# Kernel tuning notes

Measured on AMD Instinct MI355X. Metric: run time of the kernel, lower is better.

## Reference

```python
import jax, jax.numpy as jnp
import numpy as np

B, T, D, E = 8, 2048, 256, 4
D_E = D // E


def setup_inputs() -> dict:
    key = jax.random.key(0)
    ks = jax.random.split(key, 12)
    s = 1.0 / np.sqrt(D)
    x = jax.random.normal(ks[0], (B, T, D), dtype=jnp.float32)
    # ensure max(seq_len) == T so the padded input matches this_batch_padlen
    seq_len = jnp.concatenate([
        jax.random.randint(ks[1], (B - 1,), T // 2, T),
        jnp.array([T]),
    ]).astype(jnp.int32)
    return {
        "x": x,
        "seq_len": seq_len,
        "wq": jax.random.uniform(ks[2], (D, D), jnp.float32, -s, s),
        "bq": jax.random.uniform(ks[3], (D,), jnp.float32, -s, s),
        "wk": jax.random.uniform(ks[4], (D, D), jnp.float32, -s, s),
        "bk": jax.random.uniform(ks[5], (D,), jnp.float32, -s, s),
        "wv": jax.random.uniform(ks[6], (D, D), jnp.float32, -s, s),
        "bv": jax.random.uniform(ks[7], (D,), jnp.float32, -s, s),
        "wo": jax.random.uniform(ks[8], (D, D), jnp.float32, -s, s),
        "bo": jax.random.uniform(ks[9], (D,), jnp.float32, -s, s),
        "theta": jnp.array([50.0], dtype=jnp.float32),
    }


def _split_heads(y):
    # faithful to torch: [B,T,D] -> permute(0,2,1) -> [B,D,T] -> reshape(B*E, T, D_E)
    return jnp.transpose(y, (0, 2, 1)).reshape(B * E, T, D_E)


def reference(x, seq_len, wq, bq, wk, bk, wv, bv, wo, bo, theta):
    Q = _split_heads(x @ wq.T + bq)          # [B*E, T, D_E]
    K = _split_heads(x @ wk.T + bk)          # [B*E, T, D_E]
    V = _split_heads(x @ wv.T + bv)          # [B*E, T, D_E]

    # padding mask: zero out query rows (and key cols) past seq_len[i]
    pos = jnp.arange(T)
    valid = (pos[None, :] < seq_len[:, None])                 # [B, T]
    mask_q = jnp.repeat(valid, E, axis=0).astype(Q.dtype)     # [B*E, T]
    Q = Q * mask_q[:, :, None]
    K = K * mask_q[:, :, None]

    scale = jnp.sqrt(jnp.float32(T))
    att = jnp.einsum('bqd,bkd->bqk', Q, K) / scale            # [B*E, T, T]

    # Gaussian positional penalty (is_punish=True)
    tpos = jnp.arange(T, dtype=jnp.float32)
    diff = tpos[None, :] - tpos[:, None]                      # j - i
    punish = jnp.exp(-(diff ** 2) / (theta[0] ** 2))          # [T, T]
    att = att * punish[None, :, :]

    att = jnp.where(att == 0.0, jnp.float32(-2e20), att)
    att = jax.nn.softmax(att, axis=2)

    ctx = jnp.einsum('bqk,bkd->bqd', att, V)                  # [B*E, T, D_E]
    # faithful inverse of _split_heads: permute(0,2,1)->reshape(B,D,T)->permute
    ctx = jnp.transpose(jnp.transpose(ctx, (0, 2, 1)).reshape(B, D, T), (0, 2, 1))
    A = ctx @ wo.T + bo
    return A + x
```

## Files before the change

### kernel.cpp

```cpp
#include <hip/hip_runtime.h>
#include <math.h>
#include <stdint.h>

#define B_SZ   8
#define T_SEQ  2048
#define DIM    256
#define NH     32
#define DE     64
#define BAND   509
#define M_ROWS (B_SZ * T_SEQ)

typedef __attribute__((ext_vector_type(8))) short short8;
typedef __attribute__((ext_vector_type(4))) float floatx4;
typedef unsigned short ushort_t;

__device__ __forceinline__ ushort_t f2bf(float x) {
    unsigned u = __float_as_uint(x);
    u += 0x7fffu + ((u >> 16) & 1u);
    return (ushort_t)(u >> 16);
}
__device__ __forceinline__ float bf2f(ushort_t b) {
    return __uint_as_float(((unsigned)b) << 16);
}
__device__ __forceinline__ unsigned pack2(float a, float b) {
    return (unsigned)f2bf(a) | ((unsigned)f2bf(b) << 16);
}

__device__ __forceinline__ double pd_exact(int d, float th) {
    float df  = (float)d;
    float arg = (-(df * df)) / (th * th);
    double pdd = exp((double)arg);
    if (pdd < 1.17549435082228751e-38)
        return rint(pdd * 0x1p149) * 0x1p-149;
    return (double)(float)pdd;
}

__global__ __launch_bounds__(256) void prep_kernel(
    const float* __restrict__ x,
    const float* __restrict__ wq, const float* __restrict__ wk,
    const float* __restrict__ wv, const float* __restrict__ wo,
    const float* __restrict__ theta,
    ushort_t* __restrict__ xb, ushort_t* __restrict__ wb,
    float* __restrict__ thr_g, float* __restrict__ pdf_g)
{
    const int bid = blockIdx.x, tid = threadIdx.x;
    if (bid < 2048) {
        size_t i8 = ((size_t)bid * 256 + tid) * 8;
        float4 a = *(const float4*)(x + i8);
        float4 b = *(const float4*)(x + i8 + 4);
        uint4 o;
        o.x = pack2(a.x, a.y); o.y = pack2(a.z, a.w);
        o.z = pack2(b.x, b.y); o.w = pack2(b.z, b.w);
        *(uint4*)(xb + i8) = o;
    } else if (bid < 2176) {
        size_t w8 = ((size_t)(bid - 2048) * 256 + tid) * 8;
        int which = (int)(w8 >> 16);
        const float* src = (which == 0) ? wq : (which == 1) ? wk : (which == 2) ? wv : wo;
        size_t off = w8 & 65535;
        float4 a = *(const float4*)(src + off);
        float4 b = *(const float4*)(src + off + 4);
        uint4 o;
        o.x = pack2(a.x, a.y); o.y = pack2(a.z, a.w);
        o.z = pack2(b.x, b.y); o.w = pack2(b.z, b.w);
        *(uint4*)(wb + w8) = o;
    } else {
        int i = (bid - 2176) * 256 + tid;
        float th = theta[0];
        if (i < 384) pdf_g[i] = (float)pd_exact(i, th);
        if (i < 288) {
            double pdv = pd_exact(321 + i, th);
            thr_g[i] = (pdv == 0.0) ? __builtin_inff() : (float)(0x1p-150 / pdv);
        }
    }
}

__global__ __launch_bounds__(256, 2) void proj_qkv_mfma(
    const ushort_t* __restrict__ xb, const ushort_t* __restrict__ wb,
    const float* __restrict__ bq, const float* __restrict__ bk,
    const float* __restrict__ bv, const int* __restrict__ seq_len,
    ushort_t* __restrict__ Qh, ushort_t* __restrict__ Kh, ushort_t* __restrict__ Vh)
{
    __shared__ __align__(16) ushort_t Ls[4][64][68];
    const int wave = threadIdx.x >> 6, lane = threadIdx.x & 63;
    const int quad = lane >> 4, l15 = lane & 15;
    const int task = blockIdx.x * 4 + wave;
    const int nt64 = task % 12;
    const int mstrip = task / 12;
    const int mode = nt64 >> 2;
    const int nloc_base = (nt64 & 3) * 64;
    const ushort_t* Wp = wb + (size_t)mode * 65536;
    const int m0 = mstrip * 64;
    const int bb = m0 >> 11;
    const int th0 = (m0 >> 6) & 31;
    const int sl = seq_len[bb];
    ushort_t* outp = (mode == 0) ? Qh : (mode == 1) ? Kh : Vh;
    const float* bias = (mode == 0) ? bq : (mode == 1) ? bk : bv;
    const int hh = bb * 4 + (nloc_base >> 6);
    const float oscale = (mode == 0) ? 0.022097086912079612f : 1.0f;

    short8 Bf[4][8];
    #pragma unroll
    for (int nt = 0; nt < 4; ++nt) {
        int nrow = nloc_base + nt * 16 + l15;
        #pragma unroll
        for (int ks = 0; ks < 8; ++ks)
            Bf[nt][ks] = *(const short8*)(Wp + (size_t)nrow * 256 + ks * 32 + quad * 8);
    }
    float bias4[4];
    #pragma unroll
    for (int nt = 0; nt < 4; ++nt) bias4[nt] = bias[nloc_base + nt * 16 + l15];

    short8 Acur[8];
    #pragma unroll
    for (int ks = 0; ks < 8; ++ks)
        Acur[ks] = *(const short8*)(xb + (size_t)(m0 + l15) * 256 + ks * 32 + quad * 8);

    #pragma unroll
    for (int mb = 0; mb < 4; ++mb) {
        const int mb0 = m0 + mb * 16;
        short8 Anext[8];
        if (mb < 3) {
            #pragma unroll
            for (int ks = 0; ks < 8; ++ks)
                Anext[ks] = *(const short8*)(xb + (size_t)(mb0 + 16 + l15) * 256 + ks * 32 + quad * 8);
        }
        floatx4 acc[4];
        #pragma unroll
        for (int nt = 0; nt < 4; ++nt) acc[nt] = (floatx4){0.f, 0.f, 0.f, 0.f};
        #pragma unroll
        for (int ks = 0; ks < 8; ++ks)
            #pragma unroll
            for (int nt = 0; nt < 4; ++nt)
                acc[nt] = __builtin_amdgcn_mfma_f32_16x16x32_bf16(Acur[ks], Bf[nt][ks], acc[nt], 0, 0, 0);
        #pragma unroll
        for (int nt = 0; nt < 4; ++nt) {
            float v0 = (acc[nt][0] + bias4[nt]) * oscale;
            float v1 = (acc[nt][1] + bias4[nt]) * oscale;
            float v2 = (acc[nt][2] + bias4[nt]) * oscale;
            float v3 = (acc[nt][3] + bias4[nt]) * oscale;
            uint2 pk; pk.x = pack2(v0, v1); pk.y = pack2(v2, v3);
            *(uint2*)&Ls[wave][nt * 16 + l15][mb * 16 + quad * 4] = pk;
        }
        #pragma unroll
        for (int ks = 0; ks < 8; ++ks) Acur[ks] = Anext[ks];
    }

    #pragma unroll
    for (int s = 0; s < 16; ++s) {
        int dl = s * 4 + quad;
        int e0 = l15 * 4;
        uint2 pk = *(const uint2*)&Ls[wave][dl][e0];
        int q = dl * 32 + th0;
        if (mode <= 1 && q >= sl) { pk.x = 0u; pk.y = 0u; }
        *(uint2*)(outp + (((size_t)hh * T_SEQ + q) << 6) + e0) = pk;
    }
}

__global__ __launch_bounds__(256) void vtrans_kernel(const ushort_t* __restrict__ Vh,
                                                     ushort_t* __restrict__ VTp)
{
    __shared__ ushort_t Vs[256][66];
    const int tid = threadIdx.x;
    const int h = blockIdx.x >> 3, chunk = blockIdx.x & 7;
    const ushort_t* src = Vh + ((size_t)(h * T_SEQ + chunk * 256)) * DE;
    #pragma unroll
    for (int rep = 0; rep < 8; ++rep) {
        int f = rep * 256 + tid;
        int row = f >> 3, c8 = (f & 7) * 8;
        *(uint4*)&Vs[row][c8] = *(const uint4*)(src + (size_t)row * DE + c8);
    }
    __syncthreads();
    const int w = tid >> 6, lane = tid & 63;
    const int half = lane >> 5;
    const int c32 = lane & 31;
    const int cbase = c32 * 8;
    const int blk = cbase >> 6;
    const int cin = cbase & 63;
    #pragma unroll
    for (int rr = 0; rr < 8; ++rr) {
        int e = w * 16 + rr * 2 + half;
        ushort_t tmp[8];
        #pragma unroll
        for (int t = 0; t < 8; ++t) {
            int ci = cin + t;
            int j = blk * 64 + (ci >> 2) + 16 * (ci & 3);
            tmp[t] = Vs[j][e];
        }
        *(uint4*)(VTp + ((size_t)(h * DE + e)) * T_SEQ + chunk * 256 + cbase) = *(uint4*)tmp;
    }
}

__global__ __launch_bounds__(256) void meanv_partial(const ushort_t* __restrict__ Vh,
                                                     float* __restrict__ mv) {
    __shared__ float red[32][72];
    const int blk = blockIdx.x;
    const int h = blk >> 3, chunk = blk & 7;
    const int tid = threadIdx.x;
    const int r0 = tid >> 3;
    const int es = (tid & 7) * 8;
    const ushort_t* p = Vh + ((size_t)h * T_SEQ + chunk * 256 + r0) * DE + es;
    float s[8] = {};
    #pragma unroll
    for (int k = 0; k < 8; ++k) {
        uint4 u = *(const uint4*)(p + (size_t)k * 32 * DE);
        const ushort_t* w = (const ushort_t*)&u;
        #pragma unroll
        for (int i = 0; i < 8; ++i) s[i] += bf2f(w[i]);
    }
    #pragma unroll
    for (int i = 0; i < 8; ++i) red[r0][es + i] = s[i];
    __syncthreads();
    if (tid < 64) {
        float t = 0.f;
        #pragma unroll
        for (int g = 0; g < 32; ++g) t += red[g][tid];
        atomicAdd(&mv[h * DE + tid], t);
    }
}

__global__ __launch_bounds__(256) void attn_mfma_kernel(
    const ushort_t* __restrict__ Qh, const ushort_t* __restrict__ Kh,
    const ushort_t* __restrict__ VTp, const float* __restrict__ thr_g,
    const float* __restrict__ pdf_g, const float* __restrict__ mvs,
    const int* __restrict__ seq_len, ushort_t* __restrict__ ctxb)
{
    __shared__ ushort_t Ks [64][72];
    __shared__ ushort_t VTs[64][72];
    __shared__ ushort_t Ps [4][16][72];
    __shared__ float pdfs[384];
    __shared__ float thrs[288];

    const int tid  = threadIdx.x;
    const int wave = tid >> 6;
    const int lane = tid & 63;
    const int quad = lane >> 4;
    const int l15  = lane & 15;
    const int bid   = blockIdx.x;
    const int inner = bid >> 3;
    const int h  = ((inner >> 5) << 3) | (bid & 7);
    const int q0 = (inner & 31) * 64;
    const int b  = h >> 2;
    const int sl = seq_len[b];
    const float invT = 1.0f / (float)T_SEQ;
    ushort_t* outbase = ctxb + ((size_t)b * T_SEQ + q0) * DIM + (size_t)(h & 3) * 64;

    if (q0 >= sl) {
        #pragma unroll
        for (int nt = 0; nt < 4; ++nt) {
            ushort_t mval = f2bf(mvs[h * DE + l15 + 16 * nt] * invT);
            #pragma unroll
            for (int r = 0; r < 4; ++r)
                outbase[(size_t)(wave * 16 + quad * 4 + r) * DIM + l15 + 16 * nt] = mval;
        }
        return;
    }

    for (int i = tid; i < 384; i += 256) pdfs[i] = pdf_g[i];
    for (int i = tid; i < 288; i += 256) thrs[i] = thr_g[i];

    short8 qa0, qa1;
    {
        const ushort_t* qp = Qh + ((size_t)h * T_SEQ + q0 + wave * 16 + l15) * DE + quad * 8;
        qa0 = *(const short8*)(qp);
        qa1 = *(const short8*)(qp + 32);
    }

    float l_acc[4] = {0.f, 0.f, 0.f, 0.f};
    floatx4 cacc[4];
    #pragma unroll
    for (int nt = 0; nt < 4; ++nt) cacc[nt] = (floatx4){0.f, 0.f, 0.f, 0.f};

    int jlo = q0 - BAND;      if (jlo < 0) jlo = 0;
    int jhi = q0 + 63 + BAND; if (jhi > sl - 1) jhi = sl - 1;
    const int jt0 = jlo >> 6, jt1 = jhi >> 6;

    const int krow = tid >> 3;
    const int kc8  = (tid & 7) * 8;
    const ushort_t* Kbp = Kh + (size_t)h * T_SEQ * DE;
    const ushort_t* Vbp = VTp + (size_t)h * DE * T_SEQ;
    uint4 kpre0, kpre1, vpre0, vpre1;
    {
        const int j0 = jt0 << 6;
        kpre0 = *(const uint4*)(Kbp + (size_t)(j0 + krow) * DE + kc8);
        kpre1 = *(const uint4*)(Kbp + (size_t)(j0 + krow + 32) * DE + kc8);
        vpre0 = *(const uint4*)(Vbp + (size_t)krow * T_SEQ + j0 + kc8);
        vpre1 = *(const uint4*)(Vbp + (size_t)(krow + 32) * T_SEQ + j0 + kc8);
    }

    for (int jt = jt0; jt <= jt1; ++jt) {
        const int j0 = jt << 6;
        __syncthreads();
        *(uint4*)&Ks[krow][kc8]       = kpre0;
        *(uint4*)&Ks[krow + 32][kc8]  = kpre1;
        *(uint4*)&VTs[krow][kc8]      = vpre0;
        *(uint4*)&VTs[krow + 32][kc8] = vpre1;
        __syncthreads();
        if (jt < jt1) {
            const int jn = j0 + 64;
            kpre0 = *(const uint4*)(Kbp + (size_t)(jn + krow) * DE + kc8);
            kpre1 = *(const uint4*)(Kbp + (size_t)(jn + krow + 32) * DE + kc8);
            vpre0 = *(const uint4*)(Vbp + (size_t)krow * T_SEQ + jn + kc8);
            vpre1 = *(const uint4*)(Vbp + (size_t)(krow + 32) * T_SEQ + jn + kc8);
        }

        floatx4 S[4];
        #pragma unroll
        for (int nt = 0; nt < 4; ++nt) {
            short8 kb0 = *(const short8*)&Ks[l15 + 16 * nt][quad * 8];
            short8 kb1 = *(const short8*)&Ks[l15 + 16 * nt][32 + quad * 8];
            floatx4 z = {0.f, 0.f, 0.f, 0.f};
            z = __builtin_amdgcn_mfma_f32_16x16x32_bf16(qa0, kb0, z, 0, 0, 0);
            z = __builtin_amdgcn_mfma_f32_16x16x32_bf16(qa1, kb1, z, 0, 0, 0);
            S[nt] = z;
        }

        const int off = j0 - q0;
        float p[4][4];
        if (off >= -320 && off <= 320) {
            #pragma unroll
            for (int nt = 0; nt < 4; ++nt) {
                int jg = j0 + l15 + 16 * nt;
                bool jv = (jg < sl);
                #pragma unroll
                for (int r = 0; r < 4; ++r) {
                    int dd = jg - (q0 + wave * 16 + quad * 4 + r);
                    dd = dd < 0 ? -dd : dd;
                    float av = S[nt][r] * pdfs[dd];
                    av = jv ? av : -1e30f;
                    p[nt][r] = __expf(av);
                }
            }
        } else {
            #pragma unroll
            for (int nt = 0; nt < 4; ++nt) {
                int jg = j0 + l15 + 16 * nt;
                #pragma unroll
                for (int r = 0; r < 4; ++r) {
                    int dd = jg - (q0 + wave * 16 + quad * 4 + r);
                    dd = dd < 0 ? -dd : dd;
                    p[nt][r] = (fabsf(S[nt][r]) > thrs[dd - 321]) ? 1.0f : 0.0f;
                }
            }
        }

        #pragma unroll
        for (int r = 0; r < 4; ++r) {
            l_acc[r] += (p[0][r] + p[1][r]) + (p[2][r] + p[3][r]);
            uint2 pk;
            pk.x = pack2(p[0][r], p[1][r]);
            pk.y = pack2(p[2][r], p[3][r]);
            *(uint2*)&Ps[wave][quad * 4 + r][l15 * 4] = pk;
        }
        short8 pa0 = *(const short8*)&Ps[wave][l15][quad * 8];
        short8 pa1 = *(const short8*)&Ps[wave][l15][32 + quad * 8];
        #pragma unroll
        for (int nt = 0; nt < 4; ++nt) {
            short8 vb0 = *(const short8*)&VTs[l15 + 16 * nt][quad * 8];
            short8 vb1 = *(const short8*)&VTs[l15 + 16 * nt][32 + quad * 8];
            floatx4 c = cacc[nt];
            c = __builtin_amdgcn_mfma_f32_16x16x32_bf16(pa0, vb0, c, 0, 0, 0);
            c = __builtin_amdgcn_mfma_f32_16x16x32_bf16(pa1, vb1, c, 0, 0, 0);
            cacc[nt] = c;
        }
    }

    #pragma unroll
    for (int r = 0; r < 4; ++r) {
        float lv = l_acc[r];
        #pragma unroll
        for (int o = 1; o <= 8; o <<= 1) lv += __shfl_xor(lv, o);
        l_acc[r] = 1.0f / lv;
    }
    #pragma unroll
    for (int nt = 0; nt < 4; ++nt) {
        #pragma unroll
        for (int r = 0; r < 4; ++r) {
            int row = wave * 16 + quad * 4 + r;
            int qg = q0 + row;
            float o = cacc[nt][r] * l_acc[r];
            if (qg >= sl) o = mvs[h * DE + l15 + 16 * nt] * invT;
            outbase[(size_t)row * DIM + l15 + 16 * nt] = f2bf(o);
        }
    }
}

__global__ __launch_bounds__(256, 2) void proj_o_mfma(
    const ushort_t* __restrict__ ctx, const ushort_t* __restrict__ wb,
    const float* __restrict__ bo, const float* __restrict__ x,
    float* __restrict__ out)
{
    const int wave = threadIdx.x >> 6, lane = threadIdx.x & 63;
    const int quad = lane >> 4, l15 = lane & 15;
    const int task = blockIdx.x * 4 + wave;
    const int nt64 = task & 3;
    const int mstrip = task >> 2;
    const int n0 = nt64 * 64;
    const ushort_t* Wp = wb + (size_t)3 * 65536;
    const int m0 = mstrip * 64;

    short8 Bf[4][8];
    #pragma unroll
    for (int nt = 0; nt < 4; ++nt) {
        int nrow = n0 + nt * 16 + l15;
        #pragma unroll
        for (int ks = 0; ks < 8; ++ks)
            Bf[nt][ks] = *(const short8*)(Wp + (size_t)nrow * 256 + ks * 32 + quad * 8);
    }
    float bias4[4];
    #pragma unroll
    for (int nt = 0; nt < 4; ++nt) bias4[nt] = bo[n0 + nt * 16 + l15];

    short8 Acur[8];
    #pragma unroll
    for (int ks = 0; ks < 8; ++ks)
        Acur[ks] = *(const short8*)(ctx + (size_t)(m0 + l15) * 256 + ks * 32 + quad * 8);

    #pragma unroll
    for (int mb = 0; mb < 4; ++mb) {
        const int mb0 = m0 + mb * 16;
        short8 Anext[8];
        if (mb < 3) {
            #pragma unroll
            for (int ks = 0; ks < 8; ++ks)
                Anext[ks] = *(const short8*)(ctx + (size_t)(mb0 + 16 + l15) * 256 + ks * 32 + quad * 8);
        }
        floatx4 acc[4];
        #pragma unroll
        for (int nt = 0; nt < 4; ++nt) acc[nt] = (floatx4){0.f, 0.f, 0.f, 0.f};
        #pragma unroll
        for (int ks = 0; ks < 8; ++ks)
            #pragma unroll
            for (int nt = 0; nt < 4; ++nt)
                acc[nt] = __builtin_amdgcn_mfma_f32_16x16x32_bf16(Acur[ks], Bf[nt][ks], acc[nt], 0, 0, 0);
        #pragma unroll
        for (int nt = 0; nt < 4; ++nt) {
            int d = n0 + nt * 16 + l15;
            #pragma unroll
            for (int r = 0; r < 4; ++r) {
                size_t mi = (size_t)(mb0 + quad * 4 + r) * 256 + d;
                out[mi] = acc[nt][r] + bias4[nt] + x[mi];
            }
        }
        #pragma unroll
        for (int ks = 0; ks < 8; ++ks) Acur[ks] = Anext[ks];
    }
}

extern "C" void kernel_launch(void* const* d_in, const int* in_sizes, int n_in,
                              void* d_out, int out_size, void* d_ws, size_t ws_size,
                              hipStream_t stream)
{
    (void)in_sizes; (void)n_in; (void)out_size; (void)ws_size;
    const float* x  = (const float*)d_in[0];
    const int*   sl = (const int*)d_in[1];
    const float* wq = (const float*)d_in[2];
    const float* bq = (const float*)d_in[3];
    const float* wk = (const float*)d_in[4];
    const float* bk = (const float*)d_in[5];
    const float* wv = (const float*)d_in[6];
    const float* bv = (const float*)d_in[7];
    const float* wo = (const float*)d_in[8];
    const float* bo = (const float*)d_in[9];
    const float* th = (const float*)d_in[10];
    float* out = (float*)d_out;

    char* ws = (char*)d_ws;
    const size_t SZH = (size_t)M_ROWS * DIM * sizeof(ushort_t);
    ushort_t* xb  = (ushort_t*)(ws);
    ushort_t* wb  = (ushort_t*)(ws + SZH);
    ushort_t* Qh  = (ushort_t*)(ws + SZH + 524288);
    ushort_t* Kh  = (ushort_t*)(ws + 2*SZH + 524288);
    ushort_t* Vh  = (ushort_t*)(ws + 3*SZH + 524288);
    ushort_t* VTp = (ushort_t*)(ws + 4*SZH + 524288);
    ushort_t* Cb  = (ushort_t*)(ws + 5*SZH + 524288);
    float*    Mv  = (float*)   (ws + 6*SZH + 524288);
    float*    Thr = (float*)   (ws + 6*SZH + 524288 + 8192);
    float*    Pdf = (float*)   (ws + 6*SZH + 524288 + 12288);

    hipMemsetAsync(Mv, 0, NH * DE * sizeof(float), stream);
    prep_kernel<<<dim3(2178), dim3(256), 0, stream>>>(x, wq, wk, wv, wo, th, xb, wb, Thr, Pdf);
    proj_qkv_mfma<<<dim3(768), dim3(256), 0, stream>>>(xb, wb, bq, bk, bv, sl, Qh, Kh, Vh);
    vtrans_kernel<<<dim3(NH * 8), dim3(256), 0, stream>>>(Vh, VTp);
    meanv_partial<<<dim3(256), dim3(256), 0, stream>>>(Vh, Mv);
    attn_mfma_kernel<<<dim3(1024), dim3(256), 0, stream>>>(Qh, Kh, VTp, Thr, Pdf, Mv, sl, Cb);
    proj_o_mfma<<<dim3(256), dim3(256), 0, stream>>>(Cb, wb, bo, x, out);
}
```

Measured before the change: 186.6 us.

## Fuse mean-V into vtrans, shrink attention blocks, regrid projections for XCD locality

Removes the memset and the separate meanv kernel by zeroing the accumulator in prep and computing column sums of V inside the transpose kernel from shared memory. The attention kernel moves to 128-thread blocks covering 32 queries each, doubling the grid and adjusting band bounds and the K/V staging loops. The QKV projection remaps block indices so that each XCD handles contiguous row strips, and the output projection uses one 16-row tile per block with 4 blocks per CU. These aim at better occupancy, fewer launches and better L2 locality, at the cost of reloading K/V more often per query.

```diff
diff --git a/kernel.cpp b/kernel.cpp
--- a/kernel.cpp
+++ b/kernel.cpp
@@ -41,7 +41,8 @@
     const float* __restrict__ wv, const float* __restrict__ wo,
     const float* __restrict__ theta,
     ushort_t* __restrict__ xb, ushort_t* __restrict__ wb,
-    float* __restrict__ thr_g, float* __restrict__ pdf_g)
+    float* __restrict__ thr_g, float* __restrict__ pdf_g,
+    float* __restrict__ mv)
 {
     const int bid = blockIdx.x, tid = threadIdx.x;
     if (bid < 2048) {
@@ -71,6 +72,11 @@
             double pdv = pd_exact(321 + i, th);
             thr_g[i] = (pdv == 0.0) ? __builtin_inff() : (float)(0x1p-150 / pdv);
         }
+        if (bid == 2176) {
+            float4 z = {0.f, 0.f, 0.f, 0.f};
+            *(float4*)(mv + tid * 8)     = z;
+            *(float4*)(mv + tid * 8 + 4) = z;
+        }
     }
 }
 
@@ -83,9 +89,10 @@
     __shared__ __align__(16) ushort_t Ls[4][64][68];
     const int wave = threadIdx.x >> 6, lane = threadIdx.x & 63;
     const int quad = lane >> 4, l15 = lane & 15;
-    const int task = blockIdx.x * 4 + wave;
-    const int nt64 = task % 12;
-    const int mstrip = task / 12;
+    const int xcd = blockIdx.x & 7;
+    const int idx = blockIdx.x >> 3;
+    const int mstrip = xcd * 32 + idx / 3;
+    const int nt64 = (idx % 3) * 4 + wave;
     const int mode = nt64 >> 2;
     const int nloc_base = (nt64 & 3) * 64;
     const ushort_t* Wp = wb + (size_t)mode * 65536;
@@ -157,7 +164,8 @@
 }
 
 __global__ __launch_bounds__(256) void vtrans_kernel(const ushort_t* __restrict__ Vh,
-                                                     ushort_t* __restrict__ VTp)
+                                                     ushort_t* __restrict__ VTp,
+                                                     float* __restrict__ mv)
 {
     __shared__ ushort_t Vs[256][66];
     const int tid = threadIdx.x;
@@ -170,6 +178,13 @@
         *(uint4*)&Vs[row][c8] = *(const uint4*)(src + (size_t)row * DE + c8);
     }
     __syncthreads();
+    {
+        const int e = tid & 63, grp = tid >> 6;
+        float s = 0.f;
+        #pragma unroll
+        for (int k = 0; k < 64; ++k) s += bf2f(Vs[grp * 64 + k][e]);
+        atomicAdd(&mv[h * DE + e], s);
+    }
     const int w = tid >> 6, lane = tid & 63;
     const int half = lane >> 5;
     const int c32 = lane & 31;
@@ -190,35 +205,7 @@
     }
 }
 
-__global__ __launch_bounds__(256) void meanv_partial(const ushort_t* __restrict__ Vh,
-                                                     float* __restrict__ mv) {
-    __shared__ float red[32][72];
-    const int blk = blockIdx.x;
-    const int h = blk >> 3, chunk = blk & 7;
-    const int tid = threadIdx.x;
-    const int r0 = tid >> 3;
-    const int es = (tid & 7) * 8;
-    const ushort_t* p = Vh + ((size_t)h * T_SEQ + chunk * 256 + r0) * DE + es;
-    float s[8] = {};
-    #pragma unroll
-    for (int k = 0; k < 8; ++k) {
-        uint4 u = *(const uint4*)(p + (size_t)k * 32 * DE);
-        const ushort_t* w = (const ushort_t*)&u;
-        #pragma unroll
-        for (int i = 0; i < 8; ++i) s[i] += bf2f(w[i]);
-    }
-    #pragma unroll
-    for (int i = 0; i < 8; ++i) red[r0][es + i] = s[i];
-    __syncthreads();
-    if (tid < 64) {
-        float t = 0.f;
-        #pragma unroll
-        for (int g = 0; g < 32; ++g) t += red[g][tid];
-        atomicAdd(&mv[h * DE + tid], t);
-    }
-}
-
-__global__ __launch_bounds__(256) void attn_mfma_kernel(
+__global__ __launch_bounds__(128) void attn_mfma_kernel(
     const ushort_t* __restrict__ Qh, const ushort_t* __restrict__ Kh,
     const ushort_t* __restrict__ VTp, const float* __restrict__ thr_g,
     const float* __restrict__ pdf_g, const float* __restrict__ mvs,
@@ -226,7 +213,7 @@
 {
     __shared__ ushort_t Ks [64][72];
     __shared__ ushort_t VTs[64][72];
-    __shared__ ushort_t Ps [4][16][72];
+    __shared__ ushort_t Ps [2][16][72];
     __shared__ float pdfs[384];
     __shared__ float thrs[288];
 
@@ -237,8 +224,8 @@
     const int l15  = lane & 15;
     const int bid   = blockIdx.x;
     const int inner = bid >> 3;
-    const int h  = ((inner >> 5) << 3) | (bid & 7);
-    const int q0 = (inner & 31) * 64;
+    const int h  = ((inner >> 6) << 3) | (bid & 7);
+    const int q0 = (inner & 63) * 32;
     const int b  = h >> 2;
     const int sl = seq_len[b];
     const float invT = 1.0f / (float)T_SEQ;
@@ -255,8 +242,8 @@
         return;
     }
 
-    for (int i = tid; i < 384; i += 256) pdfs[i] = pdf_g[i];
-    for (int i = tid; i < 288; i += 256) thrs[i] = thr_g[i];
+    for (int i = tid; i < 384; i += 128) pdfs[i] = pdf_g[i];
+    for (int i = tid; i < 288; i += 128) thrs[i] = thr_g[i];
 
     short8 qa0, qa1;
     {
@@ -271,36 +258,39 @@
     for (int nt = 0; nt < 4; ++nt) cacc[nt] = (floatx4){0.f, 0.f, 0.f, 0.f};
 
     int jlo = q0 - BAND;      if (jlo < 0) jlo = 0;
-    int jhi = q0 + 63 + BAND; if (jhi > sl - 1) jhi = sl - 1;
+    int jhi = q0 + 31 + BAND; if (jhi > sl - 1) jhi = sl - 1;
     const int jt0 = jlo >> 6, jt1 = jhi >> 6;
 
     const int krow = tid >> 3;
     const int kc8  = (tid & 7) * 8;
     const ushort_t* Kbp = Kh + (size_t)h * T_SEQ * DE;
     const ushort_t* Vbp = VTp + (size_t)h * DE * T_SEQ;
-    uint4 kpre0, kpre1, vpre0, vpre1;
+    uint4 kpre[4], vpre[4];
     {
         const int j0 = jt0 << 6;
-        kpre0 = *(const uint4*)(Kbp + (size_t)(j0 + krow) * DE + kc8);
-        kpre1 = *(const uint4*)(Kbp + (size_t)(j0 + krow + 32) * DE + kc8);
-        vpre0 = *(const uint4*)(Vbp + (size_t)krow * T_SEQ + j0 + kc8);
-        vpre1 = *(const uint4*)(Vbp + (size_t)(krow + 32) * T_SEQ + j0 + kc8);
+        #pragma unroll
+        for (int s = 0; s < 4; ++s) {
+            kpre[s] = *(const uint4*)(Kbp + (size_t)(j0 + krow + 16 * s) * DE + kc8);
+            vpre[s] = *(const uint4*)(Vbp + (size_t)(krow + 16 * s) * T_SEQ + j0 + kc8);
+        }
     }
 
     for (int jt = jt0; jt <= jt1; ++jt) {
         const int j0 = jt << 6;
         __syncthreads();
-        *(uint4*)&Ks[krow][kc8]       = kpre0;
-        *(uint4*)&Ks[krow + 32][kc8]  = kpre1;
-        *(uint4*)&VTs[krow][kc8]      = vpre0;
-        *(uint4*)&VTs[krow + 32][kc8] = vpre1;
+        #pragma unroll
+        for (int s = 0; s < 4; ++s) {
+            *(uint4*)&Ks [krow + 16 * s][kc8] = kpre[s];
+            *(uint4*)&VTs[krow + 16 * s][kc8] = vpre[s];
+        }
         __syncthreads();
         if (jt < jt1) {
             const int jn = j0 + 64;
-            kpre0 = *(const uint4*)(Kbp + (size_t)(jn + krow) * DE + kc8);
-            kpre1 = *(const uint4*)(Kbp + (size_t)(jn + krow + 32) * DE + kc8);
-            vpre0 = *(const uint4*)(Vbp + (size_t)krow * T_SEQ + jn + kc8);
-            vpre1 = *(const uint4*)(Vbp + (size_t)(krow + 32) * T_SEQ + jn + kc8);
+            #pragma unroll
+            for (int s = 0; s < 4; ++s) {
+                kpre[s] = *(const uint4*)(Kbp + (size_t)(jn + krow + 16 * s) * DE + kc8);
+                vpre[s] = *(const uint4*)(Vbp + (size_t)(krow + 16 * s) * T_SEQ + jn + kc8);
+            }
         }
 
         floatx4 S[4];
@@ -316,7 +306,7 @@
 
         const int off = j0 - q0;
         float p[4][4];
-        if (off >= -320 && off <= 320) {
+        if (off >= -352 && off <= 320) {
             #pragma unroll
             for (int nt = 0; nt < 4; ++nt) {
                 int jg = j0 + l15 + 16 * nt;
@@ -384,19 +374,21 @@
     }
 }
 
-__global__ __launch_bounds__(256, 2) void proj_o_mfma(
+__global__ __launch_bounds__(256, 4) void proj_o_mfma(
     const ushort_t* __restrict__ ctx, const ushort_t* __restrict__ wb,
     const float* __restrict__ bo, const float* __restrict__ x,
     float* __restrict__ out)
 {
     const int wave = threadIdx.x >> 6, lane = threadIdx.x & 63;
     const int quad = lane >> 4, l15 = lane & 15;
-    const int task = blockIdx.x * 4 + wave;
-    const int nt64 = task & 3;
-    const int mstrip = task >> 2;
-    const int n0 = nt64 * 64;
+    const int n0 = wave * 64;
+    const int mb0 = blockIdx.x * 16;
     const ushort_t* Wp = wb + (size_t)3 * 65536;
-    const int m0 = mstrip * 64;
+
+    short8 Acur[8];
+    #pragma unroll
+    for (int ks = 0; ks < 8; ++ks)
+        Acur[ks] = *(const short8*)(ctx + (size_t)(mb0 + l15) * 256 + ks * 32 + quad * 8);
 
     short8 Bf[4][8];
     #pragma unroll
@@ -410,39 +402,22 @@
     #pragma unroll
     for (int nt = 0; nt < 4; ++nt) bias4[nt] = bo[n0 + nt * 16 + l15];
 
-    short8 Acur[8];
+    floatx4 acc[4];
+    #pragma unroll
+    for (int nt = 0; nt < 4; ++nt) acc[nt] = (floatx4){0.f, 0.f, 0.f, 0.f};
     #pragma unroll
     for (int ks = 0; ks < 8; ++ks)
-        Acur[ks] = *(const short8*)(ctx + (size_t)(m0 + l15) * 256 + ks * 32 + quad * 8);
-
-    #pragma unroll
-    for (int mb = 0; mb < 4; ++mb) {
-        const int mb0 = m0 + mb * 16;
-        short8 Anext[8];
-        if (mb < 3) {
-            #pragma unroll
-            for (int ks = 0; ks < 8; ++ks)
-                Anext[ks] = *(const short8*)(ctx + (size_t)(mb0 + 16 + l15) * 256 + ks * 32 + quad * 8);
-        }
-        floatx4 acc[4];
-        #pragma unroll
-        for (int nt = 0; nt < 4; ++nt) acc[nt] = (floatx4){0.f, 0.f, 0.f, 0.f};
-        #pragma unroll
-        for (int ks = 0; ks < 8; ++ks)
-            #pragma unroll
-            for (int nt = 0; nt < 4; ++nt)
-                acc[nt] = __builtin_amdgcn_mfma_f32_16x16x32_bf16(Acur[ks], Bf[nt][ks], acc[nt], 0, 0, 0);
-        #pragma unroll
-        for (int nt = 0; nt < 4; ++nt) {
-            int d = n0 + nt * 16 + l15;
-            #pragma unroll
-            for (int r = 0; r < 4; ++r) {
-                size_t mi = (size_t)(mb0 + quad * 4 + r) * 256 + d;
-                out[mi] = acc[nt][r] + bias4[nt] + x[mi];
-            }
-        }
-        #pragma unroll
-        for (int ks = 0; ks < 8; ++ks) Acur[ks] = Anext[ks];
+        #pragma unroll
+        for (int nt = 0; nt < 4; ++nt)
+            acc[nt] = __builtin_amdgcn_mfma_f32_16x16x32_bf16(Acur[ks], Bf[nt][ks], acc[nt], 0, 0, 0);
+    #pragma unroll
+    for (int nt = 0; nt < 4; ++nt) {
+        int d = n0 + nt * 16 + l15;
+        #pragma unroll
+        for (int r = 0; r < 4; ++r) {
+            size_t mi = (size_t)(mb0 + quad * 4 + r) * 256 + d;
+            out[mi] = acc[nt][r] + bias4[nt] + x[mi];
+        }
     }
 }
 
@@ -477,11 +452,9 @@
     float*    Thr = (float*)   (ws + 6*SZH + 524288 + 8192);
     float*    Pdf = (float*)   (ws + 6*SZH + 524288 + 12288);
 
-    hipMemsetAsync(Mv, 0, NH * DE * sizeof(float), stream);
-    prep_kernel<<<dim3(2178), dim3(256), 0, stream>>>(x, wq, wk, wv, wo, th, xb, wb, Thr, Pdf);
+    prep_kernel<<<dim3(2178), dim3(256), 0, stream>>>(x, wq, wk, wv, wo, th, xb, wb, Thr, Pdf, Mv);
     proj_qkv_mfma<<<dim3(768), dim3(256), 0, stream>>>(xb, wb, bq, bk, bv, sl, Qh, Kh, Vh);
-    vtrans_kernel<<<dim3(NH * 8), dim3(256), 0, stream>>>(Vh, VTp);
-    meanv_partial<<<dim3(256), dim3(256), 0, stream>>>(Vh, Mv);
-    attn_mfma_kernel<<<dim3(1024), dim3(256), 0, stream>>>(Qh, Kh, VTp, Thr, Pdf, Mv, sl, Cb);
-    proj_o_mfma<<<dim3(256), dim3(256), 0, stream>>>(Cb, wb, bo, x, out);
-}
+    vtrans_kernel<<<dim3(NH * 8), dim3(256), 0, stream>>>(Vh, VTp, Mv);
+    attn_mfma_kernel<<<dim3(2048), dim3(128), 0, stream>>>(Qh, Kh, VTp, Thr, Pdf, Mv, sl, Cb);
+    proj_o_mfma<<<dim3(1024), dim3(256), 0, stream>>>(Cb, wb, bo, x, out);
+}
```

New measurement: 284.0 us. 52.2% more time.
